# Performance work log

Hardware: AMD Instinct MI355X
Metric: run time of the kernel (lower is better)

## Reference

```python
import jax, jax.numpy as jnp
import numpy as np

INPUT_DIM = 512
EMBED_DIM = 64
B, S = 4, 4096


def setup_inputs() -> dict:
    key = jax.random.key(0)
    ks = jax.random.split(key, 9)
    scale = 1.0 / np.sqrt(INPUT_DIM)
    return {
        "q": jax.random.normal(ks[0], (B, S, INPUT_DIM), dtype=jnp.float32),
        "k": jax.random.normal(ks[1], (B, S, INPUT_DIM), dtype=jnp.float32),
        "v": jax.random.normal(ks[2], (B, S, INPUT_DIM), dtype=jnp.float32),
        "Wq": jax.random.uniform(ks[3], (INPUT_DIM, EMBED_DIM), jnp.float32, -scale, scale),
        "bq": jax.random.uniform(ks[4], (EMBED_DIM,), jnp.float32, -scale, scale),
        "Wk": jax.random.uniform(ks[5], (INPUT_DIM, EMBED_DIM), jnp.float32, -scale, scale),
        "bk": jax.random.uniform(ks[6], (EMBED_DIM,), jnp.float32, -scale, scale),
        "Wv": jax.random.uniform(ks[7], (INPUT_DIM, EMBED_DIM), jnp.float32, -scale, scale),
        "bv": jax.random.uniform(ks[8], (EMBED_DIM,), jnp.float32, -scale, scale),
    }


def reference(q, k, v, Wq, bq, Wk, bk, Wv, bv):
    # Linear projections (torch Linear: x @ W^T + b; here W stored as [in, out])
    Q = q @ Wq + bq  # [B, S, E]
    K = k @ Wk + bk  # [B, S, E]
    V = v @ Wv + bv  # [B, S, E]
    d_k = K.shape[-1]
    scores = jnp.einsum("bqe,bke->bqk", Q, K) / jnp.sqrt(jnp.float32(d_k))  # [B, S, S]
    attn = jax.nn.softmax(scores, axis=-1)
    return jnp.einsum("bqk,bke->bqe", attn, V)  # [B, S, E]
```

## Files before the change

### kernel.cpp

```cpp
#include <hip/hip_runtime.h>
#include <math.h>

#define S_ 4096
#define C_SCALE 0.18033688011112042f
#define KSPLIT 4

typedef __attribute__((ext_vector_type(4))) float  floatx4;
typedef __attribute__((ext_vector_type(4))) short  short4_t;
typedef __attribute__((ext_vector_type(8))) short  short8_t;

__device__ __forceinline__ short f2bf(float f) {
  unsigned u = __builtin_bit_cast(unsigned, f);
  u += 0x7FFFu + ((u >> 16) & 1u);
  return (short)(u >> 16);
}

__global__ __launch_bounds__(256) void prep_w(const float* __restrict__ Wq,
                                              const float* __restrict__ Wk,
                                              const float* __restrict__ Wv,
                                              short* __restrict__ Wt) {
  __shared__ float T[64 * 65];
  int m = blockIdx.x >> 3, kt = blockIdx.x & 7, tid = threadIdx.x;
  const float* W = (m == 0) ? Wq : (m == 1) ? Wk : Wv;
  float sc = (m == 0) ? C_SCALE : 1.0f;
#pragma unroll
  for (int i = 0; i < 16; i++) {
    int e = i * 256 + tid;
    int k = e >> 6, n = e & 63;
    T[k * 65 + n] = W[(kt * 64 + k) * 64 + n];
  }
  __syncthreads();
#pragma unroll
  for (int i = 0; i < 16; i++) {
    int e = i * 256 + tid;
    int n = e >> 6, k = e & 63;
    Wt[m * 32768 + n * 512 + kt * 64 + k] = f2bf(T[k * 65 + n] * sc);
  }
}

__global__ __launch_bounds__(256, 3) void proj_kernel(
    const float* __restrict__ qin, const float* __restrict__ kin,
    const float* __restrict__ vin, const float* __restrict__ bq,
    const float* __restrict__ bk, const float* __restrict__ bv,
    const short* __restrict__ Wt, short* __restrict__ Qp,
    short* __restrict__ Kp, short* __restrict__ Vt) {
  int tid = threadIdx.x;
  int m = blockIdx.x >> 8;
  int r0 = (blockIdx.x & 255) * 64;
  int wid = tid >> 6, lane = tid & 63, l15 = lane & 15, quad = lane >> 4;

  const float* in = (m == 0) ? qin : (m == 1) ? kin : vin;
  const float* abase = in + (size_t)(r0 + wid * 16 + l15) * 512 + quad * 8;
  const short* wbase = Wt + m * 32768 + l15 * 512 + quad * 8;

  floatx4 acc[4];
#pragma unroll
  for (int nb = 0; nb < 4; nb++) acc[nb] = (floatx4){0.f, 0.f, 0.f, 0.f};

  floatx4 ca[4];
  short8_t cw[8];
#pragma unroll
  for (int j = 0; j < 2; j++) {
    ca[j * 2 + 0] = *(const floatx4*)(abase + j * 32);
    ca[j * 2 + 1] = *(const floatx4*)(abase + j * 32 + 4);
  }
#pragma unroll
  for (int nb = 0; nb < 4; nb++)
#pragma unroll
    for (int kh = 0; kh < 2; kh++)
      cw[nb * 2 + kh] = *(const short8_t*)(wbase + nb * 8192 + kh * 32);

#pragma unroll
  for (int kc = 0; kc < 8; kc++) {
    floatx4 na[4];
    short8_t nw[8];
    if (kc < 7) {
#pragma unroll
      for (int j = 0; j < 2; j++) {
        na[j * 2 + 0] = *(const floatx4*)(abase + (kc + 1) * 64 + j * 32);
        na[j * 2 + 1] = *(const floatx4*)(abase + (kc + 1) * 64 + j * 32 + 4);
      }
#pragma unroll
      for (int nb = 0; nb < 4; nb++)
#pragma unroll
        for (int kh = 0; kh < 2; kh++)
          nw[nb * 2 + kh] =
              *(const short8_t*)(wbase + nb * 8192 + (kc + 1) * 64 + kh * 32);
    }
    short8_t af0 = {f2bf(ca[0][0]), f2bf(ca[0][1]), f2bf(ca[0][2]), f2bf(ca[0][3]),
                    f2bf(ca[1][0]), f2bf(ca[1][1]), f2bf(ca[1][2]), f2bf(ca[1][3])};
    short8_t af1 = {f2bf(ca[2][0]), f2bf(ca[2][1]), f2bf(ca[2][2]), f2bf(ca[2][3]),
                    f2bf(ca[3][0]), f2bf(ca[3][1]), f2bf(ca[3][2]), f2bf(ca[3][3])};
#pragma unroll
    for (int nb = 0; nb < 4; nb++) {
      acc[nb] = __builtin_amdgcn_mfma_f32_16x16x32_bf16(af0, cw[nb * 2], acc[nb], 0, 0, 0);
      acc[nb] = __builtin_amdgcn_mfma_f32_16x16x32_bf16(af1, cw[nb * 2 + 1], acc[nb], 0, 0, 0);
    }
    if (kc < 7) {
#pragma unroll
      for (int j = 0; j < 4; j++) ca[j] = na[j];
#pragma unroll
      for (int j = 0; j < 8; j++) cw[j] = nw[j];
    }
  }

  const float* bias = (m == 0) ? bq : (m == 1) ? bk : bv;
  float bsc = (m == 0) ? C_SCALE : 1.0f;
  if (m < 2) {
    short* out = (m == 0) ? Qp : Kp;
#pragma unroll
    for (int nb = 0; nb < 4; nb++) {
      float bv_ = bias[nb * 16 + l15] * bsc;
#pragma unroll
      for (int r = 0; r < 4; r++)
        out[(size_t)(r0 + wid * 16 + quad * 4 + r) * 64 + nb * 16 + l15] =
            f2bf(acc[nb][r] + bv_);
    }
  } else {
    int bb = r0 >> 12;
    int s0 = (r0 & 4095) + wid * 16 + quad * 4;
#pragma unroll
    for (int nb = 0; nb < 4; nb++) {
      float bv_ = bias[nb * 16 + l15];
      short4_t pk = {f2bf(acc[nb][0] + bv_), f2bf(acc[nb][1] + bv_),
                     f2bf(acc[nb][2] + bv_), f2bf(acc[nb][3] + bv_)};
      *(short4_t*)(Vt + (size_t)bb * 262144 + (nb * 16 + l15) * 4096 + s0) = pk;
    }
  }
}

__global__ __launch_bounds__(256, 4) void attn_kernel(
    const short* __restrict__ Qp, const short* __restrict__ Kp,
    const short* __restrict__ Vt, float* __restrict__ Po,
    float* __restrict__ Lp) {
  __shared__ short K_lds[64 * 64];
  __shared__ short V_lds[64 * 64];
  __shared__ short P_lds[4 * 16 * 64];

  int tid = threadIdx.x;
  int ks = blockIdx.x >> 8, b = (blockIdx.x >> 6) & 3, qt = blockIdx.x & 63;
  int wid = tid >> 6, lane = tid & 63, l15 = lane & 15, quad = lane >> 4;
  int xr = l15 & 7;

  const short* Qb = Qp + (size_t)b * (S_ * 64);
  const short* Kb = Kp + (size_t)b * (S_ * 64);
  const short* Vb = Vt + (size_t)b * (64 * S_);

  int q0 = qt * 64 + wid * 16;
  short8_t qf0 = *(const short8_t*)(Qb + (q0 + l15) * 64 + quad * 8);
  short8_t qf1 = *(const short8_t*)(Qb + (q0 + l15) * 64 + 32 + quad * 8);

  floatx4 o[4];
#pragma unroll
  for (int eb = 0; eb < 4; eb++) o[eb] = (floatx4){0.f, 0.f, 0.f, 0.f};
  float l_acc = 0.f;
  short* Pw = P_lds + wid * 1024;

  int sr = tid >> 3, sc16 = tid & 7;
  int swk = ((sc16 ^ (sr & 7)) * 8);
  short8_t kr0, kr1, vr0, vr1;

  int ks_base = ks * 1024;
  {
    int ks0 = ks_base;
    kr0 = *(const short8_t*)(Kb + (ks0 + sr) * 64 + sc16 * 8);
    kr1 = *(const short8_t*)(Kb + (ks0 + sr + 32) * 64 + sc16 * 8);
    vr0 = *(const short8_t*)(Vb + sr * 4096 + ks0 + sc16 * 8);
    vr1 = *(const short8_t*)(Vb + (sr + 32) * 4096 + ks0 + sc16 * 8);
  }

  for (int t = 0; t < 16; t++) {
    __syncthreads();
    *(short8_t*)(K_lds + sr * 64 + swk) = kr0;
    *(short8_t*)(K_lds + (sr + 32) * 64 + swk) = kr1;
    *(short8_t*)(V_lds + sr * 64 + swk) = vr0;
    *(short8_t*)(V_lds + (sr + 32) * 64 + swk) = vr1;
    __syncthreads();

    if (t < 15) {
      int ks0 = ks_base + (t + 1) * 64;
      kr0 = *(const short8_t*)(Kb + (ks0 + sr) * 64 + sc16 * 8);
      kr1 = *(const short8_t*)(Kb + (ks0 + sr + 32) * 64 + sc16 * 8);
      vr0 = *(const short8_t*)(Vb + sr * 4096 + ks0 + sc16 * 8);
      vr1 = *(const short8_t*)(Vb + (sr + 32) * 4096 + ks0 + sc16 * 8);
    }

    floatx4 st[4];
#pragma unroll
    for (int jb = 0; jb < 4; jb++) {
      const short* kp = K_lds + (jb * 16 + l15) * 64;
      short8_t k0 = *(const short8_t*)(kp + ((quad ^ xr) * 8));
      short8_t k1 = *(const short8_t*)(kp + (((quad + 4) ^ xr) * 8));
      floatx4 z = (floatx4){0.f, 0.f, 0.f, 0.f};
      z = __builtin_amdgcn_mfma_f32_16x16x32_bf16(k0, qf0, z, 0, 0, 0);
      st[jb] = __builtin_amdgcn_mfma_f32_16x16x32_bf16(k1, qf1, z, 0, 0, 0);
    }

    float lp = 0.f;
#pragma unroll
    for (int jb = 0; jb < 4; jb++) {
      float e0 = exp2f(st[jb][0]), e1 = exp2f(st[jb][1]);
      float e2 = exp2f(st[jb][2]), e3 = exp2f(st[jb][3]);
      lp += (e0 + e1) + (e2 + e3);
      short4_t pk = {f2bf(e0), f2bf(e1), f2bf(e2), f2bf(e3)};
      *(short4_t*)(Pw + l15 * 64 + (((2 * jb + (quad >> 1)) ^ xr) * 8) +
                   (quad & 1) * 4) = pk;
    }
    l_acc += lp;

#pragma unroll
    for (int ks2 = 0; ks2 < 2; ks2++) {
      short8_t pf = *(const short8_t*)(Pw + l15 * 64 + (((ks2 * 4 + quad) ^ xr) * 8));
#pragma unroll
      for (int eb = 0; eb < 4; eb++) {
        short8_t vf = *(const short8_t*)(V_lds + (eb * 16 + l15) * 64 +
                                         (((ks2 * 4 + quad) ^ xr) * 8));
        o[eb] = __builtin_amdgcn_mfma_f32_16x16x32_bf16(pf, vf, o[eb], 0, 0, 0);
      }
    }
  }

  l_acc += __shfl_xor(l_acc, 16, 64);
  l_acc += __shfl_xor(l_acc, 32, 64);

  int grow0 = b * 4096 + q0 + quad * 4;
  size_t pbase = (size_t)(ks * 16384 + grow0) * 64;
#pragma unroll
  for (int r = 0; r < 4; r++)
#pragma unroll
    for (int eb = 0; eb < 4; eb++)
      Po[pbase + (size_t)r * 64 + eb * 16 + l15] = o[eb][r];
  if (quad == 0) Lp[ks * 16384 + b * 4096 + q0 + l15] = l_acc;
}

__global__ __launch_bounds__(256) void combine_kernel(
    const float* __restrict__ Po, const float* __restrict__ Lp,
    float* __restrict__ out) {
  int gid = blockIdx.x * 256 + threadIdx.x;
  int grow = gid >> 4, e0 = (gid & 15) * 4;
  floatx4 s = (floatx4){0.f, 0.f, 0.f, 0.f};
  float l = 0.f;
#pragma unroll
  for (int ks = 0; ks < KSPLIT; ks++) {
    s += *(const floatx4*)(Po + (size_t)(ks * 16384 + grow) * 64 + e0);
    l += Lp[ks * 16384 + grow];
  }
  float inv = 1.0f / l;
  *(floatx4*)(out + (size_t)grow * 64 + e0) = s * inv;
}

extern "C" void kernel_launch(void* const* d_in, const int* in_sizes, int n_in,
                              void* d_out, int out_size, void* d_ws, size_t ws_size,
                              hipStream_t stream) {
  const float* q = (const float*)d_in[0];
  const float* k = (const float*)d_in[1];
  const float* v = (const float*)d_in[2];
  const float* Wq = (const float*)d_in[3];
  const float* bq = (const float*)d_in[4];
  const float* Wk = (const float*)d_in[5];
  const float* bk = (const float*)d_in[6];
  const float* Wv = (const float*)d_in[7];
  const float* bv = (const float*)d_in[8];

  char* ws = (char*)d_ws;
  short* Qp = (short*)(ws);
  short* Kp = (short*)(ws + (1u << 21));
  short* Vt = (short*)(ws + (2u << 21));
  short* Wt = (short*)(ws + (3u << 21));
  float* Po = (float*)(ws + (4u << 21));
  float* Lp = (float*)(ws + (12u << 21));

  prep_w<<<24, 256, 0, stream>>>(Wq, Wk, Wv, Wt);
  proj_kernel<<<768, 256, 0, stream>>>(q, k, v, bq, bk, bv, Wt, Qp, Kp, Vt);
  attn_kernel<<<1024, 256, 0, stream>>>(Qp, Kp, Vt, Po, Lp);
  combine_kernel<<<1024, 256, 0, stream>>>(Po, Lp, (float*)d_out);
}
```

Baseline: 186.9 us.

## Stage tiles via global_load_lds DMA and enlarge attention query tile per wave

The projection kernel now double-buffers input and weight tiles into shared memory with direct global-to-LDS loads and converts to bf16 with a cheaper perm-based pack. The attention kernel has each wave handle 64 query rows instead of 16, so every K/V tile loaded into LDS is reused across four query sub-tiles. K/V are double-buffered through DMA, the split-K factor goes from 4 to 8 and the grid is halved. The intent is to cut redundant K/V traffic and register staging, at the price of more registers and LDS per block, lower occupancy, and a larger partial-output buffer for the combine step.

```diff
diff --git a/kernel.cpp b/kernel.cpp
--- a/kernel.cpp
+++ b/kernel.cpp
@@ -3,16 +3,28 @@
 
 #define S_ 4096
 #define C_SCALE 0.18033688011112042f
-#define KSPLIT 4
+#define KSPLIT 8
 
 typedef __attribute__((ext_vector_type(4))) float  floatx4;
 typedef __attribute__((ext_vector_type(4))) short  short4_t;
 typedef __attribute__((ext_vector_type(8))) short  short8_t;
+typedef __attribute__((ext_vector_type(2))) unsigned int uintx2;
+typedef __attribute__((ext_vector_type(4))) unsigned int uintx4;
 
 __device__ __forceinline__ short f2bf(float f) {
   unsigned u = __builtin_bit_cast(unsigned, f);
   u += 0x7FFFu + ((u >> 16) & 1u);
   return (short)(u >> 16);
+}
+__device__ __forceinline__ unsigned pack2(float lo, float hi) {
+  unsigned a = __builtin_bit_cast(unsigned, lo) + 0x8000u;
+  unsigned b = __builtin_bit_cast(unsigned, hi) + 0x8000u;
+  return __builtin_amdgcn_perm(b, a, 0x07060302u);
+}
+__device__ __forceinline__ void dma16(const void* g, void* l) {
+  __builtin_amdgcn_global_load_lds(
+      (const __attribute__((address_space(1))) void*)g,
+      (__attribute__((address_space(3))) void*)l, 16, 0, 0);
 }
 
 __global__ __launch_bounds__(256) void prep_w(const float* __restrict__ Wq,
@@ -44,63 +56,61 @@
     const float* __restrict__ bk, const float* __restrict__ bv,
     const short* __restrict__ Wt, short* __restrict__ Qp,
     short* __restrict__ Kp, short* __restrict__ Vt) {
+  __shared__ float A_lds[2][64 * 64];
+  __shared__ short W_lds[2][64 * 64];
+
   int tid = threadIdx.x;
   int m = blockIdx.x >> 8;
   int r0 = (blockIdx.x & 255) * 64;
   int wid = tid >> 6, lane = tid & 63, l15 = lane & 15, quad = lane >> 4;
+  int key = l15 & 7;
 
   const float* in = (m == 0) ? qin : (m == 1) ? kin : vin;
-  const float* abase = in + (size_t)(r0 + wid * 16 + l15) * 512 + quad * 8;
-  const short* wbase = Wt + m * 32768 + l15 * 512 + quad * 8;
+  const short* Wm = Wt + m * 32768;
 
   floatx4 acc[4];
 #pragma unroll
   for (int nb = 0; nb < 4; nb++) acc[nb] = (floatx4){0.f, 0.f, 0.f, 0.f};
 
-  floatx4 ca[4];
-  short8_t cw[8];
-#pragma unroll
-  for (int j = 0; j < 2; j++) {
-    ca[j * 2 + 0] = *(const floatx4*)(abase + j * 32);
-    ca[j * 2 + 1] = *(const floatx4*)(abase + j * 32 + 4);
-  }
-#pragma unroll
-  for (int nb = 0; nb < 4; nb++)
-#pragma unroll
-    for (int kh = 0; kh < 2; kh++)
-      cw[nb * 2 + kh] = *(const short8_t*)(wbase + nb * 8192 + kh * 32);
-
-#pragma unroll
+  auto stage = [&](int kc, int buf) {
+#pragma unroll
+    for (int j = 0; j < 4; j++) {
+      int slot = wid * 256 + j * 64 + lane;
+      int r = slot >> 4, c = slot & 15;
+      int gc = (c & 8) | ((c ^ r) & 7);
+      dma16(in + (size_t)(r0 + r) * 512 + kc * 64 + gc * 4,
+            (void*)&A_lds[buf][(wid * 4 + j) * 256]);
+    }
+#pragma unroll
+    for (int j = 0; j < 2; j++) {
+      int slot = wid * 128 + j * 64 + lane;
+      int r = slot >> 3, c = slot & 7;
+      int gc = (c ^ (r & 7)) * 8;
+      dma16(Wm + r * 512 + kc * 64 + gc, (void*)&W_lds[buf][(wid * 2 + j) * 512]);
+    }
+  };
+
+  stage(0, 0);
   for (int kc = 0; kc < 8; kc++) {
-    floatx4 na[4];
-    short8_t nw[8];
-    if (kc < 7) {
-#pragma unroll
-      for (int j = 0; j < 2; j++) {
-        na[j * 2 + 0] = *(const floatx4*)(abase + (kc + 1) * 64 + j * 32);
-        na[j * 2 + 1] = *(const floatx4*)(abase + (kc + 1) * 64 + j * 32 + 4);
+    __syncthreads();
+    if (kc < 7) stage(kc + 1, (kc + 1) & 1);
+    __syncthreads();
+    const float* Ab = A_lds[kc & 1];
+    const short* Wb = W_lds[kc & 1];
+    int arow = wid * 16 + l15;
+#pragma unroll
+    for (int h = 0; h < 2; h++) {
+      floatx4 a0 = *(const floatx4*)(Ab + arow * 64 + ((h * 8) | ((quad * 2) ^ key)) * 4);
+      floatx4 a1 = *(const floatx4*)(Ab + arow * 64 + ((h * 8) | ((quad * 2 + 1) ^ key)) * 4);
+      uintx4 af = {pack2(a0[0], a0[1]), pack2(a0[2], a0[3]),
+                   pack2(a1[0], a1[1]), pack2(a1[2], a1[3])};
+      short8_t afv = __builtin_bit_cast(short8_t, af);
+#pragma unroll
+      for (int nb = 0; nb < 4; nb++) {
+        short8_t wf = *(const short8_t*)(Wb + (nb * 16 + l15) * 64 +
+                                         (((h * 4 + quad) ^ key)) * 8);
+        acc[nb] = __builtin_amdgcn_mfma_f32_16x16x32_bf16(afv, wf, acc[nb], 0, 0, 0);
       }
-#pragma unroll
-      for (int nb = 0; nb < 4; nb++)
-#pragma unroll
-        for (int kh = 0; kh < 2; kh++)
-          nw[nb * 2 + kh] =
-              *(const short8_t*)(wbase + nb * 8192 + (kc + 1) * 64 + kh * 32);
-    }
-    short8_t af0 = {f2bf(ca[0][0]), f2bf(ca[0][1]), f2bf(ca[0][2]), f2bf(ca[0][3]),
-                    f2bf(ca[1][0]), f2bf(ca[1][1]), f2bf(ca[1][2]), f2bf(ca[1][3])};
-    short8_t af1 = {f2bf(ca[2][0]), f2bf(ca[2][1]), f2bf(ca[2][2]), f2bf(ca[2][3]),
-                    f2bf(ca[3][0]), f2bf(ca[3][1]), f2bf(ca[3][2]), f2bf(ca[3][3])};
-#pragma unroll
-    for (int nb = 0; nb < 4; nb++) {
-      acc[nb] = __builtin_amdgcn_mfma_f32_16x16x32_bf16(af0, cw[nb * 2], acc[nb], 0, 0, 0);
-      acc[nb] = __builtin_amdgcn_mfma_f32_16x16x32_bf16(af1, cw[nb * 2 + 1], acc[nb], 0, 0, 0);
-    }
-    if (kc < 7) {
-#pragma unroll
-      for (int j = 0; j < 4; j++) ca[j] = na[j];
-#pragma unroll
-      for (int j = 0; j < 8; j++) cw[j] = nw[j];
     }
   }
 
@@ -129,108 +139,120 @@
   }
 }
 
-__global__ __launch_bounds__(256, 4) void attn_kernel(
+__global__ __launch_bounds__(256, 2) void attn_kernel(
     const short* __restrict__ Qp, const short* __restrict__ Kp,
     const short* __restrict__ Vt, float* __restrict__ Po,
     float* __restrict__ Lp) {
-  __shared__ short K_lds[64 * 64];
-  __shared__ short V_lds[64 * 64];
-  __shared__ short P_lds[4 * 16 * 64];
+  __shared__ short K_lds[2][64 * 64];
+  __shared__ short V_lds[2][64 * 64];
+  __shared__ short P_lds[4][64 * 64];
 
   int tid = threadIdx.x;
-  int ks = blockIdx.x >> 8, b = (blockIdx.x >> 6) & 3, qt = blockIdx.x & 63;
+  int ks = blockIdx.x >> 6, b = (blockIdx.x >> 4) & 3, qt = blockIdx.x & 15;
   int wid = tid >> 6, lane = tid & 63, l15 = lane & 15, quad = lane >> 4;
-  int xr = l15 & 7;
+  int key = l15 & 7;
 
   const short* Qb = Qp + (size_t)b * (S_ * 64);
   const short* Kb = Kp + (size_t)b * (S_ * 64);
   const short* Vb = Vt + (size_t)b * (64 * S_);
 
-  int q0 = qt * 64 + wid * 16;
-  short8_t qf0 = *(const short8_t*)(Qb + (q0 + l15) * 64 + quad * 8);
-  short8_t qf1 = *(const short8_t*)(Qb + (q0 + l15) * 64 + 32 + quad * 8);
-
-  floatx4 o[4];
-#pragma unroll
-  for (int eb = 0; eb < 4; eb++) o[eb] = (floatx4){0.f, 0.f, 0.f, 0.f};
-  float l_acc = 0.f;
-  short* Pw = P_lds + wid * 1024;
-
-  int sr = tid >> 3, sc16 = tid & 7;
-  int swk = ((sc16 ^ (sr & 7)) * 8);
-  short8_t kr0, kr1, vr0, vr1;
-
-  int ks_base = ks * 1024;
-  {
-    int ks0 = ks_base;
-    kr0 = *(const short8_t*)(Kb + (ks0 + sr) * 64 + sc16 * 8);
-    kr1 = *(const short8_t*)(Kb + (ks0 + sr + 32) * 64 + sc16 * 8);
-    vr0 = *(const short8_t*)(Vb + sr * 4096 + ks0 + sc16 * 8);
-    vr1 = *(const short8_t*)(Vb + (sr + 32) * 4096 + ks0 + sc16 * 8);
-  }
-
-  for (int t = 0; t < 16; t++) {
-    __syncthreads();
-    *(short8_t*)(K_lds + sr * 64 + swk) = kr0;
-    *(short8_t*)(K_lds + (sr + 32) * 64 + swk) = kr1;
-    *(short8_t*)(V_lds + sr * 64 + swk) = vr0;
-    *(short8_t*)(V_lds + (sr + 32) * 64 + swk) = vr1;
-    __syncthreads();
-
-    if (t < 15) {
-      int ks0 = ks_base + (t + 1) * 64;
-      kr0 = *(const short8_t*)(Kb + (ks0 + sr) * 64 + sc16 * 8);
-      kr1 = *(const short8_t*)(Kb + (ks0 + sr + 32) * 64 + sc16 * 8);
-      vr0 = *(const short8_t*)(Vb + sr * 4096 + ks0 + sc16 * 8);
-      vr1 = *(const short8_t*)(Vb + (sr + 32) * 4096 + ks0 + sc16 * 8);
-    }
-
-    floatx4 st[4];
-#pragma unroll
-    for (int jb = 0; jb < 4; jb++) {
-      const short* kp = K_lds + (jb * 16 + l15) * 64;
-      short8_t k0 = *(const short8_t*)(kp + ((quad ^ xr) * 8));
-      short8_t k1 = *(const short8_t*)(kp + (((quad + 4) ^ xr) * 8));
-      floatx4 z = (floatx4){0.f, 0.f, 0.f, 0.f};
-      z = __builtin_amdgcn_mfma_f32_16x16x32_bf16(k0, qf0, z, 0, 0, 0);
-      st[jb] = __builtin_amdgcn_mfma_f32_16x16x32_bf16(k1, qf1, z, 0, 0, 0);
-    }
-
-    float lp = 0.f;
-#pragma unroll
-    for (int jb = 0; jb < 4; jb++) {
-      float e0 = exp2f(st[jb][0]), e1 = exp2f(st[jb][1]);
-      float e2 = exp2f(st[jb][2]), e3 = exp2f(st[jb][3]);
-      lp += (e0 + e1) + (e2 + e3);
-      short4_t pk = {f2bf(e0), f2bf(e1), f2bf(e2), f2bf(e3)};
-      *(short4_t*)(Pw + l15 * 64 + (((2 * jb + (quad >> 1)) ^ xr) * 8) +
-                   (quad & 1) * 4) = pk;
-    }
-    l_acc += lp;
-
-#pragma unroll
-    for (int ks2 = 0; ks2 < 2; ks2++) {
-      short8_t pf = *(const short8_t*)(Pw + l15 * 64 + (((ks2 * 4 + quad) ^ xr) * 8));
+  int q0 = qt * 256 + wid * 64;
+
+  short8_t qf[4][2];
+#pragma unroll
+  for (int qs = 0; qs < 4; qs++)
+#pragma unroll
+    for (int h = 0; h < 2; h++)
+      qf[qs][h] = *(const short8_t*)(Qb + (q0 + qs * 16 + l15) * 64 + h * 32 + quad * 8);
+
+  floatx4 o[4][4];
+#pragma unroll
+  for (int qs = 0; qs < 4; qs++)
+#pragma unroll
+    for (int eb = 0; eb < 4; eb++) o[qs][eb] = (floatx4){0.f, 0.f, 0.f, 0.f};
+  float l_acc[4] = {0.f, 0.f, 0.f, 0.f};
+  short* Pw = &P_lds[wid][0];
+  int ks_base = ks * 512;
+
+  auto stage = [&](int t, int buf) {
+    int ks0 = ks_base + t * 64;
+#pragma unroll
+    for (int j = 0; j < 2; j++) {
+      int slot = wid * 128 + j * 64 + lane;
+      int r = slot >> 3, c = slot & 7;
+      int gc = (c ^ (r & 7)) * 8;
+      dma16(Kb + (ks0 + r) * 64 + gc, (void*)&K_lds[buf][(wid * 2 + j) * 512]);
+      dma16(Vb + (size_t)r * 4096 + ks0 + gc, (void*)&V_lds[buf][(wid * 2 + j) * 512]);
+    }
+  };
+
+  stage(0, 0);
+  for (int t = 0; t < 8; t++) {
+    __syncthreads();
+    if (t < 7) stage(t + 1, (t + 1) & 1);
+    __syncthreads();
+    const short* Kt = K_lds[t & 1];
+    const short* Vl = V_lds[t & 1];
+
+#pragma unroll
+    for (int jh = 0; jh < 2; jh++) {
+      short8_t kA[4];
+#pragma unroll
+      for (int jb = 0; jb < 2; jb++)
+#pragma unroll
+        for (int eh = 0; eh < 2; eh++)
+          kA[jb * 2 + eh] = *(const short8_t*)(
+              Kt + (jh * 32 + jb * 16 + l15) * 64 + ((eh * 4 + quad) ^ key) * 8);
+
+#pragma unroll
+      for (int qs = 0; qs < 4; qs++) {
+        floatx4 z = (floatx4){0.f, 0.f, 0.f, 0.f};
+        floatx4 s0 = __builtin_amdgcn_mfma_f32_16x16x32_bf16(kA[0], qf[qs][0], z, 0, 0, 0);
+        s0 = __builtin_amdgcn_mfma_f32_16x16x32_bf16(kA[1], qf[qs][1], s0, 0, 0, 0);
+        floatx4 s1 = __builtin_amdgcn_mfma_f32_16x16x32_bf16(kA[2], qf[qs][0], z, 0, 0, 0);
+        s1 = __builtin_amdgcn_mfma_f32_16x16x32_bf16(kA[3], qf[qs][1], s1, 0, 0, 0);
+        float e00 = __builtin_amdgcn_exp2f(s0[0]), e01 = __builtin_amdgcn_exp2f(s0[1]);
+        float e02 = __builtin_amdgcn_exp2f(s0[2]), e03 = __builtin_amdgcn_exp2f(s0[3]);
+        float e10 = __builtin_amdgcn_exp2f(s1[0]), e11 = __builtin_amdgcn_exp2f(s1[1]);
+        float e12 = __builtin_amdgcn_exp2f(s1[2]), e13 = __builtin_amdgcn_exp2f(s1[3]);
+        l_acc[qs] += ((e00 + e01) + (e02 + e03)) + ((e10 + e11) + (e12 + e13));
+        int row = (qs * 16 + l15) * 64;
+        uintx2 w0 = {pack2(e00, e01), pack2(e02, e03)};
+        uintx2 w1 = {pack2(e10, e11), pack2(e12, e13)};
+        *(uintx2*)(Pw + row + ((jh * 4 + 0 + (quad >> 1)) ^ key) * 8 + (quad & 1) * 4) = w0;
+        *(uintx2*)(Pw + row + ((jh * 4 + 2 + (quad >> 1)) ^ key) * 8 + (quad & 1) * 4) = w1;
+      }
+
+      short8_t pf[4];
+#pragma unroll
+      for (int qs = 0; qs < 4; qs++)
+        pf[qs] = *(const short8_t*)(Pw + (qs * 16 + l15) * 64 +
+                                    ((jh * 4 + quad) ^ key) * 8);
 #pragma unroll
       for (int eb = 0; eb < 4; eb++) {
-        short8_t vf = *(const short8_t*)(V_lds + (eb * 16 + l15) * 64 +
-                                         (((ks2 * 4 + quad) ^ xr) * 8));
-        o[eb] = __builtin_amdgcn_mfma_f32_16x16x32_bf16(pf, vf, o[eb], 0, 0, 0);
+        short8_t vf = *(const short8_t*)(Vl + (eb * 16 + l15) * 64 +
+                                         ((jh * 4 + quad) ^ key) * 8);
+#pragma unroll
+        for (int qs = 0; qs < 4; qs++)
+          o[qs][eb] = __builtin_amdgcn_mfma_f32_16x16x32_bf16(pf[qs], vf, o[qs][eb], 0, 0, 0);
       }
     }
   }
 
-  l_acc += __shfl_xor(l_acc, 16, 64);
-  l_acc += __shfl_xor(l_acc, 32, 64);
-
-  int grow0 = b * 4096 + q0 + quad * 4;
-  size_t pbase = (size_t)(ks * 16384 + grow0) * 64;
-#pragma unroll
-  for (int r = 0; r < 4; r++)
+#pragma unroll
+  for (int qs = 0; qs < 4; qs++) {
+    float l = l_acc[qs];
+    l += __shfl_xor(l, 16, 64);
+    l += __shfl_xor(l, 32, 64);
+    int grow_base = b * 4096 + q0 + qs * 16;
+    size_t pb = ((size_t)ks * 16384 + grow_base) * 64;
 #pragma unroll
     for (int eb = 0; eb < 4; eb++)
-      Po[pbase + (size_t)r * 64 + eb * 16 + l15] = o[eb][r];
-  if (quad == 0) Lp[ks * 16384 + b * 4096 + q0 + l15] = l_acc;
+#pragma unroll
+      for (int r = 0; r < 4; r++)
+        Po[pb + (size_t)(quad * 4 + r) * 64 + eb * 16 + l15] = o[qs][eb][r];
+    if (quad == 0) Lp[ks * 16384 + grow_base + l15] = l;
+  }
 }
 
 __global__ __launch_bounds__(256) void combine_kernel(
@@ -242,11 +264,10 @@
   float l = 0.f;
 #pragma unroll
   for (int ks = 0; ks < KSPLIT; ks++) {
-    s += *(const floatx4*)(Po + (size_t)(ks * 16384 + grow) * 64 + e0);
+    s += *(const floatx4*)(Po + ((size_t)ks * 16384 + grow) * 64 + e0);
     l += Lp[ks * 16384 + grow];
   }
-  float inv = 1.0f / l;
-  *(floatx4*)(out + (size_t)grow * 64 + e0) = s * inv;
+  *(floatx4*)(out + (size_t)grow * 64 + e0) = s * (1.0f / l);
 }
 
 extern "C" void kernel_launch(void* const* d_in, const int* in_sizes, int n_in,
@@ -268,10 +289,10 @@
   short* Vt = (short*)(ws + (2u << 21));
   short* Wt = (short*)(ws + (3u << 21));
   float* Po = (float*)(ws + (4u << 21));
-  float* Lp = (float*)(ws + (12u << 21));
+  float* Lp = (float*)(ws + (20u << 21));
 
   prep_w<<<24, 256, 0, stream>>>(Wq, Wk, Wv, Wt);
   proj_kernel<<<768, 256, 0, stream>>>(q, k, v, bq, bk, bv, Wt, Qp, Kp, Vt);
-  attn_kernel<<<1024, 256, 0, stream>>>(Qp, Kp, Vt, Po, Lp);
+  attn_kernel<<<512, 256, 0, stream>>>(Qp, Kp, Vt, Po, Lp);
   combine_kernel<<<1024, 256, 0, stream>>>(Po, Lp, (float*)d_out);
 }
```

Result: faster. 172.6 us (-7.6%).
